# Kernel optimization log

Hardware: AMD Instinct MI355X
Metric: run time of the kernel (lower is better)

The kernel has to match this reference:

```python
import jax, jax.numpy as jnp
import numpy as np

N, E = 100000, 400000
ATOM_DIM, HIDDEN, LAYERS, HEADS = 74, 256, 3, 4
OUT = HIDDEN // HEADS


def setup_inputs() -> dict:
    key = jax.random.key(0)
    ks = jax.random.split(key, 12)
    s = 1.0 / np.sqrt(HIDDEN)
    return {
        'atom_feat': jax.random.normal(ks[0], (N, ATOM_DIM), jnp.float32),
        'src': jax.random.randint(ks[1], (E,), 0, N, jnp.int32),
        'dst': jax.random.randint(ks[2], (E,), 0, N, jnp.int32),
        'W_in': jax.random.normal(ks[3], (ATOM_DIM, HIDDEN), jnp.float32) / np.sqrt(ATOM_DIM),
        'b_in': jnp.zeros((HIDDEN,), jnp.float32),
        'W_src': jax.random.normal(ks[4], (LAYERS, HIDDEN, HIDDEN), jnp.float32) * s,
        'b_src': jnp.zeros((LAYERS, HIDDEN), jnp.float32),
        'W_dst': jax.random.normal(ks[5], (LAYERS, HIDDEN, HIDDEN), jnp.float32) * s,
        'b_dst': jnp.zeros((LAYERS, HIDDEN), jnp.float32),
        'attn': jax.random.normal(ks[6], (LAYERS, HEADS, OUT), jnp.float32) * s,
        'bias': jnp.zeros((LAYERS, HIDDEN), jnp.float32),
    }


def _gatv2_layer(h, src, dst, Ws, bs, Wd, bd, a, b_out):
    # h: [N, HIDDEN]; fc_src / fc_dst projections reshaped to [N, HEADS, OUT]
    fs = (h @ Ws + bs).reshape(N, HEADS, OUT)
    fd = (h @ Wd + bd).reshape(N, HEADS, OUT)
    # GATv2: e_ij = a . leaky_relu(Ws h_i + Wd h_j) per head  -> [E, HEADS]
    e = jax.nn.leaky_relu(fs[src] + fd[dst], negative_slope=0.2)
    logits = jnp.einsum('ehd,hd->eh', e, a)
    # segment softmax over incoming edges of each dst node
    m = jax.ops.segment_max(logits, dst, num_segments=N)      # [N, HEADS]
    ex = jnp.exp(logits - m[dst])
    denom = jax.ops.segment_sum(ex, dst, num_segments=N)      # [N, HEADS]
    alpha = ex / denom[dst]                                   # [E, HEADS]
    # weighted scatter-aggregate of source features -> [N, HEADS, OUT]
    msg = alpha[:, :, None] * fs[src]
    rst = jax.ops.segment_sum(msg, dst, num_segments=N)
    # flatten(1) + per-layer output bias
    return rst.reshape(N, HIDDEN) + b_out


def reference(atom_feat, src, dst, W_in, b_in, W_src, b_src, W_dst, b_dst, attn, bias):
    h = atom_feat @ W_in + b_in
    for l in range(LAYERS):
        h = _gatv2_layer(h, src, dst, W_src[l], b_src[l], W_dst[l], b_dst[l], attn[l], bias[l])
    return h  # [N, HIDDEN]; per-molecule list is just slicing of this matrix
```

## Files before the change

kernel.cpp:

```cpp
#include <hip/hip_runtime.h>
#include <hip/hip_fp16.h>

#define HID   256
#define NHEAD 4
#define DOUT  64
#define ADIM  74
#define KPAD_IN 96
#define LAYERS 3

typedef _Float16 half8 __attribute__((ext_vector_type(8)));
typedef _Float16 half4 __attribute__((ext_vector_type(4)));
typedef float f32x4 __attribute__((ext_vector_type(4)));

__device__ __forceinline__ void gload16(const void* g, void* l) {
  __builtin_amdgcn_global_load_lds((const __attribute__((address_space(1))) void*)g,
                                   (__attribute__((address_space(3))) void*)l, 16, 0, 0);
}

__global__ void k_prep_wt(const float* __restrict__ Ws, const float* __restrict__ Wd,
                          _Float16* __restrict__ WT) {
  int l = blockIdx.y;
  int id = blockIdx.x * 256 + threadIdx.x;
  if (id >= 512 * HID) return;
  int n = id >> 8, k = id & 255;
  const float* W = (n < HID) ? (Ws + (size_t)l * HID * HID)
                             : (Wd + (size_t)l * HID * HID);
  int nn = (n < HID) ? n : (n - HID);
  WT[(size_t)l * 512 * HID + id] = (_Float16)W[k * HID + nn];
}

__global__ void k_prep_win(const float* __restrict__ Win, _Float16* __restrict__ WT) {
  int id = blockIdx.x * 256 + threadIdx.x;
  if (id >= HID * KPAD_IN) return;
  int n = id / KPAD_IN, k = id % KPAD_IN;
  WT[id] = (_Float16)((k < ADIM) ? Win[k * HID + n] : 0.f);
}

__device__ __forceinline__ void gemm_epilogue2(
    f32x4 acc[4][4], char* smem, int t, int lane, int wm, int wn,
    int row0, int col0, int M,
    const float* bias0, const float* bias1,
    _Float16* outS, _Float16* outD)
{
  const float* bp = (col0 < HID) ? (bias0 + col0) : (bias1 + (col0 - HID));
  _Float16*    op = (col0 < HID) ? (outS + col0) : (outD + (col0 - HID));
  _Float16 (*C)[136] = (_Float16(*)[136])smem;
  #pragma unroll
  for (int half = 0; half < 2; ++half) {
    __syncthreads();
    if (wm == half) {
      #pragma unroll
      for (int i = 0; i < 4; ++i) {
        #pragma unroll
        for (int j = 0; j < 4; ++j) {
          int lc = wn * 64 + j * 16 + (lane & 15);
          float bv = bp[lc];
          #pragma unroll
          for (int r = 0; r < 4; ++r) {
            int lr = i * 16 + (lane >> 4) * 4 + r;
            C[lr][lc] = (_Float16)(acc[i][j][r] + bv);
          }
        }
      }
    }
    __syncthreads();
    int lr = t >> 2, seg = t & 3;
    int grow = row0 + half * 64 + lr;
    if (grow < M) {
      const _Float16* sp = &C[lr][seg * 32];
      _Float16* dp = op + (size_t)grow * HID + seg * 32;
      #pragma unroll
      for (int q = 0; q < 4; ++q)
        *(uint4*)(dp + q * 8) = *(const uint4*)(sp + q * 8);
    }
  }
}

__global__ __launch_bounds__(256)
void k_gemm_h(const _Float16* __restrict__ A, int M,
              const _Float16* __restrict__ B,
              const float* __restrict__ bias0, const float* __restrict__ bias1,
              _Float16* __restrict__ outS, _Float16* __restrict__ outD)
{
  __shared__ __align__(16) char smem[32768];
  const int t = threadIdx.x, lane = t & 63, wid = t >> 6;
  const int wm = wid >> 1, wn = wid & 1;
  const int nwg = gridDim.x, id = blockIdx.x;
  const int qc = nwg >> 3, rc = nwg & 7, xcd = id & 7, idx = id >> 3;
  const int swz = (xcd < rc ? xcd * (qc + 1) : rc * (qc + 1) + (xcd - rc) * qc) + idx;
  const int col0 = (swz & 3) * 128, row0 = (swz >> 2) * 128;

  f32x4 acc[4][4];
  #pragma unroll
  for (int i = 0; i < 4; ++i)
    #pragma unroll
    for (int j = 0; j < 4; ++j)
      acc[i][j] = (f32x4){0.f, 0.f, 0.f, 0.f};

  auto stage = [&](int kt, int buf) {
    const int kb = kt * 32;
    char* Ab = smem + buf * 16384;
    char* Bb = Ab + 8192;
    #pragma unroll
    for (int q = 0; q < 2; ++q) {
      int ci = wid * 2 + q;
      int r = ci * 16 + (lane >> 2);
      int slot = (lane & 3) ^ (r & 3);
      int grow = row0 + r; grow = grow < M ? grow : (M - 1);
      gload16(A + (size_t)grow * HID + kb + slot * 8, Ab + ci * 1024);
      gload16(B + (size_t)(col0 + r) * HID + kb + slot * 8, Bb + ci * 1024);
    }
  };

  stage(0, 0);
  __syncthreads();
  int cur = 0;
  for (int kt = 0; kt < 8; ++kt) {
    if (kt < 7) stage(kt + 1, cur ^ 1);
    const char* Ab = smem + cur * 16384;
    const char* Bb = Ab + 8192;
    half8 af[4], bf[4];
    #pragma unroll
    for (int i = 0; i < 4; ++i) {
      int r = wm * 64 + i * 16 + (lane & 15);
      int slot = (lane >> 4) ^ (r & 3);
      af[i] = *(const half8*)(Ab + r * 64 + slot * 16);
    }
    #pragma unroll
    for (int j = 0; j < 4; ++j) {
      int r = wn * 64 + j * 16 + (lane & 15);
      int slot = (lane >> 4) ^ (r & 3);
      bf[j] = *(const half8*)(Bb + r * 64 + slot * 16);
    }
    #pragma unroll
    for (int i = 0; i < 4; ++i)
      #pragma unroll
      for (int j = 0; j < 4; ++j)
        acc[i][j] = __builtin_amdgcn_mfma_f32_16x16x32_f16(af[i], bf[j], acc[i][j], 0, 0, 0);
    __syncthreads();
    cur ^= 1;
  }
  gemm_epilogue2(acc, smem, t, lane, wm, wn, row0, col0, M, bias0, bias1, outS, outD);
}

__global__ __launch_bounds__(256)
void k_gemm_f(const float* __restrict__ A, int M,
              const _Float16* __restrict__ B,
              const float* __restrict__ bias0,
              _Float16* __restrict__ outS)
{
  __shared__ __align__(16) char smem[17408];
  const int t = threadIdx.x, lane = t & 63, wid = t >> 6;
  const int wm = wid >> 1, wn = wid & 1;
  const int nwg = gridDim.x, id = blockIdx.x;
  const int qc = nwg >> 3, rc = nwg & 7, xcd = id & 7, idx = id >> 3;
  const int swz = (xcd < rc ? xcd * (qc + 1) : rc * (qc + 1) + (xcd - rc) * qc) + idx;
  const int col0 = (swz & 1) * 128, row0 = (swz >> 1) * 128;
  char* Ab = smem;
  char* Bb = smem + 8192;

  f32x4 acc[4][4];
  #pragma unroll
  for (int i = 0; i < 4; ++i)
    #pragma unroll
    for (int j = 0; j < 4; ++j)
      acc[i][j] = (f32x4){0.f, 0.f, 0.f, 0.f};

  for (int kt = 0; kt < 3; ++kt) {
    const int kb = kt * 32;
    #pragma unroll
    for (int it = 0; it < 4; ++it) {
      int idx2 = t + it * 256;
      int r = idx2 >> 3, c4 = idx2 & 7;
      int gr = row0 + r;
      int k0 = kb + c4 * 4;
      float x0 = 0.f, x1 = 0.f, x2 = 0.f, x3 = 0.f;
      if (gr < M) {
        const float* ap = A + (size_t)gr * ADIM;
        if (k0 + 0 < ADIM) x0 = ap[k0 + 0];
        if (k0 + 1 < ADIM) x1 = ap[k0 + 1];
        if (k0 + 2 < ADIM) x2 = ap[k0 + 2];
        if (k0 + 3 < ADIM) x3 = ap[k0 + 3];
      }
      half4 hv = {(_Float16)x0, (_Float16)x1, (_Float16)x2, (_Float16)x3};
      int off = r * 64 + ((c4 * 8) ^ ((r & 3) << 4));
      *(half4*)(Ab + off) = hv;
    }
    #pragma unroll
    for (int q = 0; q < 2; ++q) {
      int ci = wid * 2 + q;
      int r = ci * 16 + (lane >> 2);
      int slot = (lane & 3) ^ (r & 3);
      gload16(B + (size_t)(col0 + r) * KPAD_IN + kb + slot * 8, Bb + ci * 1024);
    }
    __syncthreads();
    half8 af[4], bf[4];
    #pragma unroll
    for (int i = 0; i < 4; ++i) {
      int r = wm * 64 + i * 16 + (lane & 15);
      int slot = (lane >> 4) ^ (r & 3);
      af[i] = *(const half8*)(Ab + r * 64 + slot * 16);
    }
    #pragma unroll
    for (int j = 0; j < 4; ++j) {
      int r = wn * 64 + j * 16 + (lane & 15);
      int slot = (lane >> 4) ^ (r & 3);
      bf[j] = *(const half8*)(Bb + r * 64 + slot * 16);
    }
    #pragma unroll
    for (int i = 0; i < 4; ++i)
      #pragma unroll
      for (int j = 0; j < 4; ++j)
        acc[i][j] = __builtin_amdgcn_mfma_f32_16x16x32_f16(af[i], bf[j], acc[i][j], 0, 0, 0);
    __syncthreads();
  }
  gemm_epilogue2(acc, smem, t, lane, wm, wn, row0, col0, M, bias0, bias0, outS, outS);
}

__global__ __launch_bounds__(256)
void k_fused(const int* __restrict__ offs, const int* __restrict__ esrc,
             const int* __restrict__ perm,
             const _Float16* __restrict__ fs, const _Float16* __restrict__ fd,
             const float* __restrict__ attn, const float* __restrict__ bias,
             _Float16* __restrict__ hhalf, float* __restrict__ hfloat, int N)
{
  int gid = blockIdx.x * 8 + (threadIdx.x >> 5);
  if (gid >= N) return;
  int n = perm[gid];
  int sub = threadIdx.x & 31;
  int h = sub >> 3;
  int j0 = sub * 8;
  half8 fdv = *(const half8*)&fd[(size_t)n * HID + j0];
  float4 av0 = *(const float4*)&attn[h * DOUT + (sub & 7) * 8];
  float4 av1 = *(const float4*)&attn[h * DOUT + (sub & 7) * 8 + 4];
  float4 bv0 = *(const float4*)&bias[j0];
  float4 bv1 = *(const float4*)&bias[j0 + 4];
  float fdf[8], avf[8], bvf[8];
  #pragma unroll
  for (int q = 0; q < 4; ++q) {
    avf[q] = ((const float*)&av0)[q]; avf[q + 4] = ((const float*)&av1)[q];
    bvf[q] = ((const float*)&bv0)[q]; bvf[q + 4] = ((const float*)&bv1)[q];
  }
  #pragma unroll
  for (int q = 0; q < 8; ++q) fdf[q] = (float)fdv[q];

  int t0 = offs[n], t1 = offs[n + 1];
  float m = -1e30f, ssum = 0.f;
  float a[8];
  #pragma unroll
  for (int q = 0; q < 8; ++q) a[q] = 0.f;

  half8 fN = {};
  if (t0 < t1) {
    int s0 = esrc[t0];
    fN = *(const half8*)&fs[(size_t)s0 * HID + j0];
  }
  for (int tt = t0; tt < t1; ++tt) {
    half8 fv = fN;
    if (tt + 1 < t1) {
      int s2 = esrc[tt + 1];
      fN = *(const half8*)&fs[(size_t)s2 * HID + j0];
    }
    float f[8];
    #pragma unroll
    for (int q = 0; q < 8; ++q) f[q] = (float)fv[q];
    float p = 0.f;
    #pragma unroll
    for (int q = 0; q < 8; ++q) {
      float x = f[q] + fdf[q];
      x = x > 0.f ? x : 0.2f * x;
      p += x * avf[q];
    }
    p += __shfl_xor(p, 1);
    p += __shfl_xor(p, 2);
    p += __shfl_xor(p, 4);
    if (p > m) {
      float sc = __expf(m - p);
      ssum = ssum * sc + 1.f;
      #pragma unroll
      for (int q = 0; q < 8; ++q) a[q] = a[q] * sc + f[q];
      m = p;
    } else {
      float w = __expf(p - m);
      ssum += w;
      #pragma unroll
      for (int q = 0; q < 8; ++q) a[q] += w * f[q];
    }
  }
  float inv = (t1 > t0) ? 1.0f / ssum : 0.f;
  float o[8];
  #pragma unroll
  for (int q = 0; q < 8; ++q) o[q] = a[q] * inv + bvf[q];
  if (hhalf) {
    half8 hv;
    #pragma unroll
    for (int q = 0; q < 8; ++q) hv[q] = (_Float16)o[q];
    *(half8*)&hhalf[(size_t)n * HID + j0] = hv;
  }
  if (hfloat) {
    float4 v0 = {o[0], o[1], o[2], o[3]};
    float4 v1 = {o[4], o[5], o[6], o[7]};
    *(float4*)&hfloat[(size_t)n * HID + j0] = v0;
    *(float4*)&hfloat[(size_t)n * HID + j0 + 4] = v1;
  }
}

__global__ void k_zero_i(int* p, int n) {
  int i = blockIdx.x * 256 + threadIdx.x;
  if (i < n) p[i] = 0;
}
__global__ void k_count(const int* __restrict__ dst, int* __restrict__ counts, int E) {
  int i = blockIdx.x * 256 + threadIdx.x;
  if (i < E) atomicAdd(&counts[dst[i]], 1);
}
__global__ __launch_bounds__(1024)
void k_scan1(const int* __restrict__ counts, int* __restrict__ offs,
             int* __restrict__ bsums, int* __restrict__ dhist, int N)
{
  __shared__ int sd[1024];
  __shared__ int hh[64];
  int t = threadIdx.x, i = blockIdx.x * 1024 + t;
  if (t < 64) hh[t] = 0;
  int x = (i < N) ? counts[i] : 0;
  sd[t] = x;
  __syncthreads();
  if (i < N) atomicAdd(&hh[x < 63 ? x : 63], 1);
  for (int off = 1; off < 1024; off <<= 1) {
    int v = (t >= off) ? sd[t - off] : 0;
    __syncthreads();
    sd[t] += v;
    __syncthreads();
  }
  if (i < N) offs[i] = sd[t] - x;
  if (t == 0) bsums[blockIdx.x] = sd[1023];
  __syncthreads();
  if (t < 64 && hh[t] > 0) atomicAdd(&dhist[t], hh[t]);
}
__global__ void k_scan2(const int* __restrict__ bsums, int* __restrict__ boffs,
                        int* __restrict__ offs, int nb, int N)
{
  if (threadIdx.x == 0 && blockIdx.x == 0) {
    int run = 0;
    for (int b = 0; b < nb; ++b) { boffs[b] = run; run += bsums[b]; }
    offs[N] = run;
  }
}
__global__ void k_deg_scan(const int* __restrict__ dhist, int* __restrict__ dcur) {
  int t = threadIdx.x;
  int x = dhist[t];
  int sum = x;
  for (int off = 1; off < 64; off <<= 1) {
    int v = __shfl_up(sum, off);
    if (t >= off) sum += v;
  }
  dcur[t] = sum - x;
}
__global__ __launch_bounds__(1024)
void k_scan3(const int* __restrict__ boffs, int* __restrict__ offs,
             int* __restrict__ cursor, int N)
{
  int i = blockIdx.x * 1024 + threadIdx.x;
  if (i < N) {
    int v = offs[i] + boffs[blockIdx.x];
    offs[i] = v;
    cursor[i] = v;
  }
}
__global__ void k_scatter(const int* __restrict__ src, const int* __restrict__ dst,
                          int* __restrict__ cursor, int* __restrict__ esrc, int E)
{
  int i = blockIdx.x * 256 + threadIdx.x;
  if (i < E) {
    int pos = atomicAdd(&cursor[dst[i]], 1);
    esrc[pos] = src[i];
  }
}
__global__ __launch_bounds__(256)
void k_deg_scatter(const int* __restrict__ counts, int* __restrict__ dcur,
                   int* __restrict__ perm, int N)
{
  __shared__ int hist[64];
  __shared__ int base[64];
  int t = threadIdx.x;
  int i = blockIdx.x * 256 + t;
  if (t < 64) hist[t] = 0;
  __syncthreads();
  int d = 0, lrank = 0;
  if (i < N) {
    d = counts[i]; d = d < 63 ? d : 63;
    lrank = atomicAdd(&hist[d], 1);
  }
  __syncthreads();
  if (t < 64 && hist[t] > 0) base[t] = atomicAdd(&dcur[t], hist[t]);
  __syncthreads();
  if (i < N) perm[base[d] + lrank] = i;
}

extern "C" void kernel_launch(void* const* d_in, const int* in_sizes, int n_in,
                              void* d_out, int out_size, void* d_ws, size_t ws_size,
                              hipStream_t stream)
{
  const float* atom  = (const float*)d_in[0];
  const int*   src   = (const int*)d_in[1];
  const int*   dst   = (const int*)d_in[2];
  const float* W_in  = (const float*)d_in[3];
  const float* b_in  = (const float*)d_in[4];
  const float* W_src = (const float*)d_in[5];
  const float* b_src = (const float*)d_in[6];
  const float* W_dst = (const float*)d_in[7];
  const float* b_dst = (const float*)d_in[8];
  const float* attn  = (const float*)d_in[9];
  const float* bias  = (const float*)d_in[10];

  const int N = in_sizes[0] / ADIM;
  const int E = in_sizes[1];
  _Float16* h_half = (_Float16*)d_out;
  float*    h_out  = (float*)d_out;

  char* w = (char*)d_ws;
  size_t off = 0;
  auto carve = [&](size_t bytes) {
    void* p = w + off;
    off = (off + bytes + 255) & ~(size_t)255;
    return p;
  };
  _Float16* fs    = (_Float16*)carve((size_t)N * HID * 2);
  _Float16* fd    = (_Float16*)carve((size_t)N * HID * 2);
  _Float16* WT    = (_Float16*)carve((size_t)LAYERS * 512 * HID * 2);
  _Float16* WTin  = (_Float16*)carve((size_t)HID * KPAD_IN * 2);
  int*      counts= (int*)carve((size_t)(N + 64) * 4);
  int*      dhist = counts + N;
  int*      offs  = (int*)carve((size_t)(N + 1) * 4);
  int*      cursor= (int*)carve((size_t)N * 4);
  int*      esrc  = (int*)carve((size_t)E * 4);
  int*      perm  = (int*)carve((size_t)N * 4);
  int*      dcur  = (int*)carve((size_t)64 * 4);
  int*      bsums = (int*)carve((size_t)1024 * 4);
  int*      boffs = (int*)carve((size_t)1024 * 4);
  (void)ws_size; (void)n_in; (void)out_size;

  const int nb = (N + 1023) / 1024;
  const int gmx = (N + 127) / 128;

  k_zero_i<<<(N + 64 + 255) / 256, 256, 0, stream>>>(counts, N + 64);
  k_count<<<(E + 255) / 256, 256, 0, stream>>>(dst, counts, E);
  k_scan1<<<nb, 1024, 0, stream>>>(counts, offs, bsums, dhist, N);
  k_scan2<<<1, 64, 0, stream>>>(bsums, boffs, offs, nb, N);
  k_deg_scan<<<1, 64, 0, stream>>>(dhist, dcur);
  k_scan3<<<nb, 1024, 0, stream>>>(boffs, offs, cursor, N);
  k_scatter<<<(E + 255) / 256, 256, 0, stream>>>(src, dst, cursor, esrc, E);
  k_deg_scatter<<<(N + 255) / 256, 256, 0, stream>>>(counts, dcur, perm, N);

  k_prep_win<<<(HID * KPAD_IN + 255) / 256, 256, 0, stream>>>(W_in, WTin);
  k_prep_wt<<<dim3((512 * HID + 255) / 256, LAYERS), 256, 0, stream>>>(W_src, W_dst, WT);
  k_gemm_f<<<2 * gmx, 256, 0, stream>>>(atom, N, WTin, b_in, h_half);

  for (int l = 0; l < LAYERS; ++l) {
    k_gemm_h<<<4 * gmx, 256, 0, stream>>>(h_half, N, WT + (size_t)l * 512 * HID,
                                          b_src + (size_t)l * HID,
                                          b_dst + (size_t)l * HID, fs, fd);
    const bool last = (l == LAYERS - 1);
    k_fused<<<(N + 7) / 8, 256, 0, stream>>>(offs, esrc, perm, fs, fd,
                                             attn + (size_t)l * NHEAD * DOUT,
                                             bias + (size_t)l * HID,
                                             last ? nullptr : h_half,
                                             last ? h_out : nullptr, N);
  }
}
```

Baseline: 487.4 us.

## Triple-buffer hidden GEMM, change LDS swizzle, unroll edge loop by two

```diff
diff --git a/kernel.cpp b/kernel.cpp
--- a/kernel.cpp
+++ b/kernel.cpp
@@ -82,7 +82,7 @@
               const float* __restrict__ bias0, const float* __restrict__ bias1,
               _Float16* __restrict__ outS, _Float16* __restrict__ outD)
 {
-  __shared__ __align__(16) char smem[32768];
+  __shared__ __align__(16) char smem[49152];
   const int t = threadIdx.x, lane = t & 63, wid = t >> 6;
   const int wm = wid >> 1, wn = wid & 1;
   const int nwg = gridDim.x, id = blockIdx.x;
@@ -104,8 +104,9 @@
     #pragma unroll
     for (int q = 0; q < 2; ++q) {
       int ci = wid * 2 + q;
-      int r = ci * 16 + (lane >> 2);
-      int slot = (lane & 3) ^ (r & 3);
+      int lr = lane >> 2;
+      int r = ci * 16 + lr;
+      int slot = (lane & 3) ^ ((lr >> 1) & 3);
       int grow = row0 + r; grow = grow < M ? grow : (M - 1);
       gload16(A + (size_t)grow * HID + kb + slot * 8, Ab + ci * 1024);
       gload16(B + (size_t)(col0 + r) * HID + kb + slot * 8, Bb + ci * 1024);
@@ -113,32 +114,37 @@
   };
 
   stage(0, 0);
-  __syncthreads();
-  int cur = 0;
+  stage(1, 1);
+  const int slot_off = (((lane >> 4) ^ ((lane >> 1) & 3)) << 4);
+  const int ar0 = (wm * 64 + (lane & 15)) * 64 + slot_off;
+  const int br0 = (wn * 64 + (lane & 15)) * 64 + slot_off;
+
+  #pragma unroll
   for (int kt = 0; kt < 8; ++kt) {
-    if (kt < 7) stage(kt + 1, cur ^ 1);
-    const char* Ab = smem + cur * 16384;
+    if (kt + 2 < 8) stage(kt + 2, (kt + 2) % 3);
+    if (kt < 6)       asm volatile("s_waitcnt vmcnt(8)" ::: "memory");
+    else if (kt == 6) asm volatile("s_waitcnt vmcnt(4)" ::: "memory");
+    else              asm volatile("s_waitcnt vmcnt(0)" ::: "memory");
+    __builtin_amdgcn_s_barrier();
+    __builtin_amdgcn_sched_barrier(0);
+    const char* Ab = smem + (kt % 3) * 16384;
     const char* Bb = Ab + 8192;
     half8 af[4], bf[4];
     #pragma unroll
-    for (int i = 0; i < 4; ++i) {
-      int r = wm * 64 + i * 16 + (lane & 15);
-      int slot = (lane >> 4) ^ (r & 3);
-      af[i] = *(const half8*)(Ab + r * 64 + slot * 16);
-    }
-    #pragma unroll
-    for (int j = 0; j < 4; ++j) {
-      int r = wn * 64 + j * 16 + (lane & 15);
-      int slot = (lane >> 4) ^ (r & 3);
-      bf[j] = *(const half8*)(Bb + r * 64 + slot * 16);
-    }
+    for (int i = 0; i < 4; ++i) af[i] = *(const half8*)(Ab + ar0 + i * 1024);
+    #pragma unroll
+    for (int j = 0; j < 4; ++j) bf[j] = *(const half8*)(Bb + br0 + j * 1024);
+    __builtin_amdgcn_s_setprio(1);
     #pragma unroll
     for (int i = 0; i < 4; ++i)
       #pragma unroll
       for (int j = 0; j < 4; ++j)
         acc[i][j] = __builtin_amdgcn_mfma_f32_16x16x32_f16(af[i], bf[j], acc[i][j], 0, 0, 0);
-    __syncthreads();
-    cur ^= 1;
+    __builtin_amdgcn_s_setprio(0);
+    asm volatile("s_waitcnt lgkmcnt(0)" ::: "memory");
+    __builtin_amdgcn_sched_barrier(0);
+    __builtin_amdgcn_s_barrier();
+    __builtin_amdgcn_sched_barrier(0);
   }
   gemm_epilogue2(acc, smem, t, lane, wm, wn, row0, col0, M, bias0, bias1, outS, outD);
 }
@@ -165,6 +171,10 @@
     #pragma unroll
     for (int j = 0; j < 4; ++j)
       acc[i][j] = (f32x4){0.f, 0.f, 0.f, 0.f};
+
+  const int slot_off = (((lane >> 4) ^ ((lane >> 1) & 3)) << 4);
+  const int ar0 = (wm * 64 + (lane & 15)) * 64 + slot_off;
+  const int br0 = (wn * 64 + (lane & 15)) * 64 + slot_off;
 
   for (int kt = 0; kt < 3; ++kt) {
     const int kb = kt * 32;
@@ -183,30 +193,23 @@
         if (k0 + 3 < ADIM) x3 = ap[k0 + 3];
       }
       half4 hv = {(_Float16)x0, (_Float16)x1, (_Float16)x2, (_Float16)x3};
-      int off = r * 64 + ((c4 * 8) ^ ((r & 3) << 4));
+      int off = r * 64 + ((((c4 >> 1) ^ ((r >> 1) & 3)) << 4)) + (c4 & 1) * 8;
       *(half4*)(Ab + off) = hv;
     }
     #pragma unroll
     for (int q = 0; q < 2; ++q) {
       int ci = wid * 2 + q;
-      int r = ci * 16 + (lane >> 2);
-      int slot = (lane & 3) ^ (r & 3);
+      int lr = lane >> 2;
+      int r = ci * 16 + lr;
+      int slot = (lane & 3) ^ ((lr >> 1) & 3);
       gload16(B + (size_t)(col0 + r) * KPAD_IN + kb + slot * 8, Bb + ci * 1024);
     }
     __syncthreads();
     half8 af[4], bf[4];
     #pragma unroll
-    for (int i = 0; i < 4; ++i) {
-      int r = wm * 64 + i * 16 + (lane & 15);
-      int slot = (lane >> 4) ^ (r & 3);
-      af[i] = *(const half8*)(Ab + r * 64 + slot * 16);
-    }
-    #pragma unroll
-    for (int j = 0; j < 4; ++j) {
-      int r = wn * 64 + j * 16 + (lane & 15);
-      int slot = (lane >> 4) ^ (r & 3);
-      bf[j] = *(const half8*)(Bb + r * 64 + slot * 16);
-    }
+    for (int i = 0; i < 4; ++i) af[i] = *(const half8*)(Ab + ar0 + i * 1024);
+    #pragma unroll
+    for (int j = 0; j < 4; ++j) bf[j] = *(const half8*)(Bb + br0 + j * 1024);
     #pragma unroll
     for (int i = 0; i < 4; ++i)
       #pragma unroll
@@ -250,42 +253,53 @@
   #pragma unroll
   for (int q = 0; q < 8; ++q) a[q] = 0.f;
 
-  half8 fN = {};
-  if (t0 < t1) {
-    int s0 = esrc[t0];
-    fN = *(const half8*)&fs[(size_t)s0 * HID + j0];
-  }
-  for (int tt = t0; tt < t1; ++tt) {
-    half8 fv = fN;
-    if (tt + 1 < t1) {
-      int s2 = esrc[tt + 1];
-      fN = *(const half8*)&fs[(size_t)s2 * HID + j0];
-    }
-    float f[8];
-    #pragma unroll
-    for (int q = 0; q < 8; ++q) f[q] = (float)fv[q];
-    float p = 0.f;
+  half8 fA = {}, fB = {};
+  if (t0 < t1)     fA = *(const half8*)&fs[(size_t)esrc[t0] * HID + j0];
+  if (t0 + 1 < t1) fB = *(const half8*)&fs[(size_t)esrc[t0 + 1] * HID + j0];
+  int tt = t0;
+  for (; tt + 1 < t1; tt += 2) {
+    float fa[8], fb[8];
+    #pragma unroll
+    for (int q = 0; q < 8; ++q) { fa[q] = (float)fA[q]; fb[q] = (float)fB[q]; }
+    if (tt + 2 < t1) fA = *(const half8*)&fs[(size_t)esrc[tt + 2] * HID + j0];
+    if (tt + 3 < t1) fB = *(const half8*)&fs[(size_t)esrc[tt + 3] * HID + j0];
+    float pa = 0.f, pb = 0.f;
     #pragma unroll
     for (int q = 0; q < 8; ++q) {
-      float x = f[q] + fdf[q];
-      x = x > 0.f ? x : 0.2f * x;
-      p += x * avf[q];
-    }
-    p += __shfl_xor(p, 1);
-    p += __shfl_xor(p, 2);
-    p += __shfl_xor(p, 4);
-    if (p > m) {
-      float sc = __expf(m - p);
-      ssum = ssum * sc + 1.f;
-      #pragma unroll
-      for (int q = 0; q < 8; ++q) a[q] = a[q] * sc + f[q];
-      m = p;
-    } else {
-      float w = __expf(p - m);
-      ssum += w;
-      #pragma unroll
-      for (int q = 0; q < 8; ++q) a[q] += w * f[q];
-    }
+      float xa = fa[q] + fdf[q]; xa = xa > 0.f ? xa : 0.2f * xa; pa += xa * avf[q];
+      float xb = fb[q] + fdf[q]; xb = xb > 0.f ? xb : 0.2f * xb; pb += xb * avf[q];
+    }
+    pa += __shfl_xor(pa, 1); pb += __shfl_xor(pb, 1);
+    pa += __shfl_xor(pa, 2); pb += __shfl_xor(pb, 2);
+    pa += __shfl_xor(pa, 4); pb += __shfl_xor(pb, 4);
+    float mx = fmaxf(m, fmaxf(pa, pb));
+    float sc = __expf(m - mx);
+    float wa = __expf(pa - mx);
+    float wb = __expf(pb - mx);
+    ssum = ssum * sc + wa + wb;
+    #pragma unroll
+    for (int q = 0; q < 8; ++q) a[q] = a[q] * sc + wa * fa[q] + wb * fb[q];
+    m = mx;
+  }
+  if (tt < t1) {
+    float fa[8];
+    #pragma unroll
+    for (int q = 0; q < 8; ++q) fa[q] = (float)fA[q];
+    float pa = 0.f;
+    #pragma unroll
+    for (int q = 0; q < 8; ++q) {
+      float xa = fa[q] + fdf[q]; xa = xa > 0.f ? xa : 0.2f * xa; pa += xa * avf[q];
+    }
+    pa += __shfl_xor(pa, 1);
+    pa += __shfl_xor(pa, 2);
+    pa += __shfl_xor(pa, 4);
+    float mx = fmaxf(m, pa);
+    float sc = __expf(m - mx);
+    float wa = __expf(pa - mx);
+    ssum = ssum * sc + wa;
+    #pragma unroll
+    for (int q = 0; q < 8; ++q) a[q] = a[q] * sc + wa * fa[q];
+    m = mx;
   }
   float inv = (t1 > t0) ? 1.0f / ssum : 0.f;
   float o[8];
```

New measurement: 459.8 us. 1.06x faster.
